# Optimization experiments

Measured on AMD Instinct MI355X. Metric: run time of the kernel, lower is better.

The kernel has to match this reference:

```python
import jax, jax.numpy as jnp
import numpy as np

N, S, C, K, V = 8, 2048, 4, 512, 64


def setup_inputs() -> dict:
    key = jax.random.key(0)
    kx, ke = jax.random.split(key)
    x = jax.random.normal(kx, (N, S, C, V), dtype=jnp.float32)
    # nn.Parameter(torch.rand(...)) -> uniform [0,1)
    embedding = jax.random.uniform(ke, (C, K, V), dtype=jnp.float32)
    return {"x": x, "embedding": embedding}


def reference(x, embedding):
    n, s, c, v = x.shape
    xf = x.reshape(n * s, c, v)  # (NS, C, V)
    x2 = jnp.sum(xf * xf, axis=-1, keepdims=True)           # (NS, C, 1)
    e2 = jnp.sum(embedding * embedding, axis=-1)            # (C, K)
    xe = jnp.einsum('ncv,ckv->nck', xf, embedding)          # (NS, C, K)
    d2 = x2 - 2.0 * xe + e2[None]                           # (NS, C, K)
    index = jnp.argmin(d2, axis=2)                          # (NS, C)
    # gather: output[n, c] = embedding[c, index[n, c]]
    output = embedding[jnp.arange(c)[None, :], index]       # (NS, C, V)
    output = output.reshape(x.shape)
    out0 = jax.lax.stop_gradient(output - x) + x            # straight-through
    d1 = jax.lax.stop_gradient(x) - output
    out1 = jnp.sum(d1 * d1, axis=3)                         # (N, S, C)
    d2_ = x - jax.lax.stop_gradient(output)
    out2 = jnp.sum(d2_ * d2_, axis=3)                       # (N, S, C)
    return (out0, out1, out2)
```

## Files before the change

kernel.cpp:

```cpp
#include <hip/hip_runtime.h>

#define NROW 16384
#define CCH  4
#define KCB  512
#define VDIM 64

typedef __attribute__((ext_vector_type(8))) short  short8;
typedef __attribute__((ext_vector_type(4))) float  floatx4;

__device__ inline unsigned short bf16h(float v, float* rem) {
    unsigned u = __float_as_uint(v);
    unsigned r = u + 0x7FFFu + ((u >> 16) & 1u);
    unsigned short h = (unsigned short)(r >> 16);
    *rem = v - __uint_as_float((unsigned)h << 16);
    return h;
}
__device__ inline unsigned short bf16r(float v) {
    unsigned u = __float_as_uint(v);
    return (unsigned short)((u + 0x7FFFu + ((u >> 16) & 1u)) >> 16);
}

__global__ __launch_bounds__(512, 4)
void vq_fused(const float* __restrict__ x, const float* __restrict__ emb,
              float* __restrict__ out) {
    extern __shared__ unsigned short smem[];
    unsigned short* eh = smem;
    float* e2s = (float*)(smem + 32768);
    float* pkm = e2s + KCB;

    const int tid  = threadIdx.x;
    const int lane = tid & 63;
    const int m    = lane & 15;
    const int quad = lane >> 4;
    const int wave = tid >> 6;
    const int c    = blockIdx.y;
    const int blockRow = blockIdx.x * 128;

    const float* embc = emb + (size_t)c * (KCB * VDIM);

    {
        const int cb = wave * 64;
        const int koct = m >> 1, half = m & 1;
#pragma unroll
        for (int j = 0; j < 16; ++j) {
            const int g = cb * 16 + j * 64 + lane;
            const float4 t = ((const float4*)embc)[g];
            const int code = cb + j * 4 + quad;
            ushort4 h4;
            h4.x = bf16r(t.x); h4.y = bf16r(t.y);
            h4.z = bf16r(t.z); h4.w = bf16r(t.w);
            const int off = (koct * 512 + (code ^ koct)) * 8 + half * 4;
            *(ushort4*)&eh[off] = h4;
            float s = 0.f;
            s = fmaf(t.x, t.x, s); s = fmaf(t.y, t.y, s);
            s = fmaf(t.z, t.z, s); s = fmaf(t.w, t.w, s);
            s += __shfl_xor(s, 1, 64);
            s += __shfl_xor(s, 2, 64);
            s += __shfl_xor(s, 4, 64);
            s += __shfl_xor(s, 8, 64);
            if (m == 0) e2s[code] = s;
        }
    }

    const int kh  = wave >> 2;
    const int rb2 = blockRow + (wave & 3) * 32;
    short8 ah[2][2], al[2][2];
#pragma unroll
    for (int rg = 0; rg < 2; ++rg) {
        const int row = rb2 + rg * 16 + m;
        const float4* xr = (const float4*)(x + ((size_t)row * CCH + c) * VDIM);
#pragma unroll
        for (int h = 0; h < 2; ++h) {
            const float4 f0 = xr[h * 8 + quad * 2];
            const float4 f1 = xr[h * 8 + quad * 2 + 1];
            const float fv[8] = {f0.x, f0.y, f0.z, f0.w, f1.x, f1.y, f1.z, f1.w};
            short8 hh, ll;
#pragma unroll
            for (int j = 0; j < 8; ++j) {
                float r, d;
                hh[j] = (short)bf16h(fv[j], &r);
                ll[j] = (short)bf16h(r, &d);
            }
            ah[rg][h] = hh; al[rg][h] = ll;
        }
    }

    __syncthreads();

    float pk0[4], pk1[4];
#pragma unroll
    for (int j = 0; j < 4; ++j) {
        pk0[j] = __uint_as_float(0x7F7FFFFFu);
        pk1[j] = __uint_as_float(0x7F7FFFFFu);
    }

    const int mq0 = m ^ quad;
    const int mq1 = m ^ (quad + 4);
    const int codeLane = kh * 256 + m;

#pragma unroll 2
    for (int t = 0; t < 16; ++t) {
        const int tt = kh * 16 + t;
        const short8 bh0 = *(const short8*)&eh[( quad      * 512 + tt * 16 + mq0) * 8];
        const short8 bh1 = *(const short8*)&eh[((quad + 4) * 512 + tt * 16 + mq1) * 8];
        const float e2v = e2s[tt * 16 + m];
        const int  code = codeLane + t * 16;

        floatx4 a0 = {0.f,0.f,0.f,0.f}, a1 = {0.f,0.f,0.f,0.f};
        a0 = __builtin_amdgcn_mfma_f32_16x16x32_bf16(ah[0][0], bh0, a0, 0, 0, 0);
        a1 = __builtin_amdgcn_mfma_f32_16x16x32_bf16(ah[1][0], bh0, a1, 0, 0, 0);
        a0 = __builtin_amdgcn_mfma_f32_16x16x32_bf16(al[0][0], bh0, a0, 0, 0, 0);
        a1 = __builtin_amdgcn_mfma_f32_16x16x32_bf16(al[1][0], bh0, a1, 0, 0, 0);
        a0 = __builtin_amdgcn_mfma_f32_16x16x32_bf16(ah[0][1], bh1, a0, 0, 0, 0);
        a1 = __builtin_amdgcn_mfma_f32_16x16x32_bf16(ah[1][1], bh1, a1, 0, 0, 0);
        a0 = __builtin_amdgcn_mfma_f32_16x16x32_bf16(al[0][1], bh1, a0, 0, 0, 0);
        a1 = __builtin_amdgcn_mfma_f32_16x16x32_bf16(al[1][1], bh1, a1, 0, 0, 0);

#pragma unroll
        for (int j = 0; j < 4; ++j) {
            const float d0 = fmaf(-2.0f, a0[j], e2v);
            pk0[j] = fminf(pk0[j],
                __uint_as_float((__float_as_uint(d0) & 0xFFFFFE00u) | code));
            const float d1 = fmaf(-2.0f, a1[j], e2v);
            pk1[j] = fminf(pk1[j],
                __uint_as_float((__float_as_uint(d1) & 0xFFFFFE00u) | code));
        }
    }

#pragma unroll
    for (int j = 0; j < 4; ++j) {
#pragma unroll
        for (int mask = 1; mask < 16; mask <<= 1) {
            pk0[j] = fminf(pk0[j], __shfl_xor(pk0[j], mask, 64));
            pk1[j] = fminf(pk1[j], __shfl_xor(pk1[j], mask, 64));
        }
    }

    {
        const int rloc = (wave & 3) * 32;
#pragma unroll
        for (int j = 0; j < 4; ++j) {
            if (m == j) {
                pkm[(rloc + quad * 4 + j) * 2 + kh]      = pk0[j];
                pkm[(rloc + 16 + quad * 4 + j) * 2 + kh] = pk1[j];
            }
        }
    }

    __syncthreads();

    const size_t base1 = (size_t)NROW * CCH * VDIM;
    const size_t base2 = base1 + (size_t)NROW * CCH;
#pragma unroll
    for (int j = 0; j < 4; ++j) {
        const int rl   = wave * 16 + quad * 4 + j;
        const float pmin = fminf(pkm[rl * 2], pkm[rl * 2 + 1]);
        const int  code  = (int)(__float_as_uint(pmin) & 511u);
        const int  row   = blockRow + rl;
        const float4 t4 = ((const float4*)(x + ((size_t)row * CCH + c) * VDIM))[m];
        const float4 e4 = ((const float4*)(embc + (size_t)code * VDIM))[m];
        float4 w;
        w.x = (e4.x - t4.x) + t4.x;
        w.y = (e4.y - t4.y) + t4.y;
        w.z = (e4.z - t4.z) + t4.z;
        w.w = (e4.w - t4.w) + t4.w;
        ((float4*)(out + ((size_t)row * CCH + c) * VDIM))[m] = w;
        float s = 0.f, dx;
        dx = t4.x - e4.x; s = fmaf(dx, dx, s);
        dx = t4.y - e4.y; s = fmaf(dx, dx, s);
        dx = t4.z - e4.z; s = fmaf(dx, dx, s);
        dx = t4.w - e4.w; s = fmaf(dx, dx, s);
        s += __shfl_xor(s, 1, 64);
        s += __shfl_xor(s, 2, 64);
        s += __shfl_xor(s, 4, 64);
        s += __shfl_xor(s, 8, 64);
        if (m == 0) {
            const size_t idx = (size_t)row * CCH + c;
            out[base1 + idx] = s;
            out[base2 + idx] = s;
        }
    }
}

extern "C" void kernel_launch(void* const* d_in, const int* in_sizes, int n_in,
                              void* d_out, int out_size, void* d_ws, size_t ws_size,
                              hipStream_t stream) {
    const float* x   = (const float*)d_in[0];
    const float* emb = (const float*)d_in[1];
    float* out = (float*)d_out;
    const size_t lds_bytes = 65536u + 2048u + 1024u;
    vq_fused<<<dim3(NROW / 128, CCH), dim3(512), lds_bytes, stream>>>(x, emb, out);
}
```

Measured before the change: 85.28 us.

## Precompute bf16 swizzled codebook and norms in a separate pre-pass kernel

Adds a small kernel that converts the embedding codebook to bf16 in the swizzled LDS layout and computes the squared norms once per channel, writing them to the workspace. The main kernel then copies the ready layout straight into LDS instead of having all 512 blocks redo the conversion and shuffle reductions. This adds a second launch and a serial dependency, and the precompute grid is only 4 blocks, which could add latency.

Result: no change. 86.47 us (+1.4%).

```diff
diff --git a/kernel.cpp b/kernel.cpp
--- a/kernel.cpp
+++ b/kernel.cpp
@@ -20,9 +20,31 @@
     return (unsigned short)((u + 0x7FFFu + ((u >> 16) & 1u)) >> 16);
 }
 
+__global__ __launch_bounds__(512)
+void vq_precomp(const float* __restrict__ emb, unsigned short* __restrict__ ws) {
+    const int c = blockIdx.x;
+    const int k = threadIdx.x;
+    const float* er = emb + ((size_t)c * KCB + k) * VDIM;
+    unsigned short* wc = ws + (size_t)c * 32768;
+    float s = 0.f;
+#pragma unroll
+    for (int q = 0; q < 16; ++q) {
+        const float4 t = ((const float4*)er)[q];
+        ushort4 h4;
+        h4.x = bf16r(t.x); h4.y = bf16r(t.y);
+        h4.z = bf16r(t.z); h4.w = bf16r(t.w);
+        const int koct = q >> 1, half = q & 1;
+        *(ushort4*)&wc[(koct * 512 + (k ^ koct)) * 8 + half * 4] = h4;
+        s = fmaf(t.x, t.x, s); s = fmaf(t.y, t.y, s);
+        s = fmaf(t.z, t.z, s); s = fmaf(t.w, t.w, s);
+    }
+    ((float*)(ws + 4 * 32768))[c * 512 + k] = s;
+}
+
+template <int MODE>
 __global__ __launch_bounds__(512, 4)
 void vq_fused(const float* __restrict__ x, const float* __restrict__ emb,
-              float* __restrict__ out) {
+              const unsigned short* __restrict__ ws, float* __restrict__ out) {
     extern __shared__ unsigned short smem[];
     unsigned short* eh = smem;
     float* e2s = (float*)(smem + 32768);
@@ -38,7 +60,13 @@
 
     const float* embc = emb + (size_t)c * (KCB * VDIM);
 
-    {
+    if constexpr (MODE == 1) {
+        const short8* wsrc = (const short8*)(ws + (size_t)c * 32768);
+#pragma unroll
+        for (int r = 0; r < 8; ++r)
+            *(short8*)&eh[(r * 512 + tid) * 8] = wsrc[r * 512 + tid];
+        e2s[tid] = ((const float*)(ws + 4 * 32768))[c * 512 + tid];
+    } else {
         const int cb = wave * 64;
         const int koct = m >> 1, half = m & 1;
 #pragma unroll
@@ -189,5 +217,14 @@
     const float* emb = (const float*)d_in[1];
     float* out = (float*)d_out;
     const size_t lds_bytes = 65536u + 2048u + 1024u;
-    vq_fused<<<dim3(NROW / 128, CCH), dim3(512), lds_bytes, stream>>>(x, emb, out);
-}
+    const size_t ws_need = 4u * 32768u * 2u + 4u * 512u * 4u;
+    if (d_ws != nullptr && ws_size >= ws_need) {
+        unsigned short* ws = (unsigned short*)d_ws;
+        vq_precomp<<<dim3(CCH), dim3(512), 0, stream>>>(emb, ws);
+        vq_fused<1><<<dim3(NROW / 128, CCH), dim3(512), lds_bytes, stream>>>(
+            x, emb, ws, out);
+    } else {
+        vq_fused<0><<<dim3(NROW / 128, CCH), dim3(512), lds_bytes, stream>>>(
+            x, emb, nullptr, out);
+    }
+}
```

## Stage reconstructed x in LDS and use nontemporal loads/stores

Applied to the files above, without the earlier changes.

Instead of re-reading x from global memory in the epilogue, the kernel rebuilds x from the bf16 hi/lo split already held in registers and stages it in LDS (padded stride) for the distance computation. The straight-through output now stores the codebook vector directly, and x loads and all output stores use nontemporal hints. This removes a second global read of x, but it adds an extra barrier and LDS traffic. The reconstructed x carries only about 16 mantissa bits, so the distance outputs may differ slightly from the fp32 reference.

Measured after the change: 104.5 us. 22.6% more time.

```diff
diff --git a/kernel.cpp b/kernel.cpp
--- a/kernel.cpp
+++ b/kernel.cpp
@@ -18,6 +18,9 @@
 __device__ inline unsigned short bf16r(float v) {
     unsigned u = __float_as_uint(v);
     return (unsigned short)((u + 0x7FFFu + ((u >> 16) & 1u)) >> 16);
+}
+__device__ inline float bf16f(short v) {
+    return __uint_as_float(((unsigned)(unsigned short)v) << 16);
 }
 
 __global__ __launch_bounds__(512, 4)
@@ -68,11 +71,11 @@
 #pragma unroll
     for (int rg = 0; rg < 2; ++rg) {
         const int row = rb2 + rg * 16 + m;
-        const float4* xr = (const float4*)(x + ((size_t)row * CCH + c) * VDIM);
+        const floatx4* xr = (const floatx4*)(x + ((size_t)row * CCH + c) * VDIM);
 #pragma unroll
         for (int h = 0; h < 2; ++h) {
-            const float4 f0 = xr[h * 8 + quad * 2];
-            const float4 f1 = xr[h * 8 + quad * 2 + 1];
+            const floatx4 f0 = __builtin_nontemporal_load(xr + h * 8 + quad * 2);
+            const floatx4 f1 = __builtin_nontemporal_load(xr + h * 8 + quad * 2 + 1);
             const float fv[8] = {f0.x, f0.y, f0.z, f0.w, f1.x, f1.y, f1.z, f1.w};
             short8 hh, ll;
 #pragma unroll
@@ -149,6 +152,31 @@
 
     __syncthreads();
 
+    {
+        floatx4* xs4 = (floatx4*)smem;
+        if (kh == 0) {
+#pragma unroll
+            for (int rg = 0; rg < 2; ++rg) {
+                const int lr = (wave & 3) * 32 + rg * 16 + m;
+#pragma unroll
+                for (int h = 0; h < 2; ++h) {
+#pragma unroll
+                    for (int hf = 0; hf < 2; ++hf) {
+                        floatx4 v;
+                        v.x = bf16f(ah[rg][h][hf * 4 + 0]) + bf16f(al[rg][h][hf * 4 + 0]);
+                        v.y = bf16f(ah[rg][h][hf * 4 + 1]) + bf16f(al[rg][h][hf * 4 + 1]);
+                        v.z = bf16f(ah[rg][h][hf * 4 + 2]) + bf16f(al[rg][h][hf * 4 + 2]);
+                        v.w = bf16f(ah[rg][h][hf * 4 + 3]) + bf16f(al[rg][h][hf * 4 + 3]);
+                        xs4[lr * 17 + h * 8 + quad * 2 + hf] = v;
+                    }
+                }
+            }
+        }
+    }
+
+    __syncthreads();
+
+    const floatx4* xs4 = (const floatx4*)smem;
     const size_t base1 = (size_t)NROW * CCH * VDIM;
     const size_t base2 = base1 + (size_t)NROW * CCH;
 #pragma unroll
@@ -157,14 +185,10 @@
         const float pmin = fminf(pkm[rl * 2], pkm[rl * 2 + 1]);
         const int  code  = (int)(__float_as_uint(pmin) & 511u);
         const int  row   = blockRow + rl;
-        const float4 t4 = ((const float4*)(x + ((size_t)row * CCH + c) * VDIM))[m];
-        const float4 e4 = ((const float4*)(embc + (size_t)code * VDIM))[m];
-        float4 w;
-        w.x = (e4.x - t4.x) + t4.x;
-        w.y = (e4.y - t4.y) + t4.y;
-        w.z = (e4.z - t4.z) + t4.z;
-        w.w = (e4.w - t4.w) + t4.w;
-        ((float4*)(out + ((size_t)row * CCH + c) * VDIM))[m] = w;
+        const floatx4 t4 = xs4[rl * 17 + m];
+        const floatx4 e4 = ((const floatx4*)(embc + (size_t)code * VDIM))[m];
+        __builtin_nontemporal_store(
+            e4, (floatx4*)(out + ((size_t)row * CCH + c) * VDIM) + m);
         float s = 0.f, dx;
         dx = t4.x - e4.x; s = fmaf(dx, dx, s);
         dx = t4.y - e4.y; s = fmaf(dx, dx, s);
@@ -176,8 +200,8 @@
         s += __shfl_xor(s, 8, 64);
         if (m == 0) {
             const size_t idx = (size_t)row * CCH + c;
-            out[base1 + idx] = s;
-            out[base2 + idx] = s;
+            __builtin_nontemporal_store(s, &out[base1 + idx]);
+            __builtin_nontemporal_store(s, &out[base2 + idx]);
         }
     }
 }
```

## Split codebook across blocks with atomicMin argmin, separate epilogue kernel

Applied to the files above, without the earlier changes.

Splits the argmin into a kernel whose grid also spans two codebook halves. Each block loads only half the embedding into LDS, halving the LDS footprint and allowing more resident blocks. Partial minima are merged with atomicMin on an order-preserving key in a workspace, and a second kernel gathers the chosen codes and writes the outputs with coalesced row-wide access. This adds a memset, two extra launches, atomic traffic and a second read of x, and falls back to the old fused kernel when no workspace is available.

After: 88.71 us. 1.04x slower.

```diff
diff --git a/kernel.cpp b/kernel.cpp
--- a/kernel.cpp
+++ b/kernel.cpp
@@ -20,13 +20,12 @@
     return (unsigned short)((u + 0x7FFFu + ((u >> 16) & 1u)) >> 16);
 }
 
-__global__ __launch_bounds__(512, 4)
-void vq_fused(const float* __restrict__ x, const float* __restrict__ emb,
-              float* __restrict__ out) {
+__global__ __launch_bounds__(512, 8)
+void vq_argmin(const float* __restrict__ x, const float* __restrict__ emb,
+               unsigned int* __restrict__ ws) {
     extern __shared__ unsigned short smem[];
     unsigned short* eh = smem;
-    float* e2s = (float*)(smem + 32768);
-    float* pkm = e2s + KCB;
+    float* e2s = (float*)(smem + 16384);
 
     const int tid  = threadIdx.x;
     const int lane = tid & 63;
@@ -34,22 +33,23 @@
     const int quad = lane >> 4;
     const int wave = tid >> 6;
     const int c    = blockIdx.y;
+    const int half = blockIdx.z;
     const int blockRow = blockIdx.x * 128;
 
-    const float* embc = emb + (size_t)c * (KCB * VDIM);
+    const float* embh = emb + ((size_t)c * KCB + (size_t)half * 256) * VDIM;
 
     {
-        const int cb = wave * 64;
-        const int koct = m >> 1, half = m & 1;
-#pragma unroll
-        for (int j = 0; j < 16; ++j) {
+        const int cb = wave * 32;
+        const int koct = m >> 1, hlf = m & 1;
+#pragma unroll
+        for (int j = 0; j < 8; ++j) {
             const int g = cb * 16 + j * 64 + lane;
-            const float4 t = ((const float4*)embc)[g];
+            const float4 t = ((const float4*)embh)[g];
             const int code = cb + j * 4 + quad;
             ushort4 h4;
             h4.x = bf16r(t.x); h4.y = bf16r(t.y);
             h4.z = bf16r(t.z); h4.w = bf16r(t.w);
-            const int off = (koct * 512 + (code ^ koct)) * 8 + half * 4;
+            const int off = (koct * 256 + (code ^ koct)) * 8 + hlf * 4;
             *(ushort4*)&eh[off] = h4;
             float s = 0.f;
             s = fmaf(t.x, t.x, s); s = fmaf(t.y, t.y, s);
@@ -62,6 +62,150 @@
         }
     }
 
+    short8 ah[2], al[2];
+    {
+        const int row = blockRow + wave * 16 + m;
+        const float4* xr = (const float4*)(x + ((size_t)row * CCH + c) * VDIM);
+#pragma unroll
+        for (int h = 0; h < 2; ++h) {
+            const float4 f0 = xr[h * 8 + quad * 2];
+            const float4 f1 = xr[h * 8 + quad * 2 + 1];
+            const float fv[8] = {f0.x, f0.y, f0.z, f0.w, f1.x, f1.y, f1.z, f1.w};
+            short8 hh, ll;
+#pragma unroll
+            for (int j = 0; j < 8; ++j) {
+                float r, d;
+                hh[j] = (short)bf16h(fv[j], &r);
+                ll[j] = (short)bf16h(r, &d);
+            }
+            ah[h] = hh; al[h] = ll;
+        }
+    }
+
+    __syncthreads();
+
+    float pk[4];
+#pragma unroll
+    for (int j = 0; j < 4; ++j) pk[j] = __uint_as_float(0x7F7FFFFFu);
+
+    const int mq0 = m ^ quad;
+    const int mq1 = m ^ (quad + 4);
+    const int codeLane = half * 256 + m;
+
+#pragma unroll 2
+    for (int t = 0; t < 16; ++t) {
+        const short8 bh0 = *(const short8*)&eh[( quad      * 256 + t * 16 + mq0) * 8];
+        const short8 bh1 = *(const short8*)&eh[((quad + 4) * 256 + t * 16 + mq1) * 8];
+        const float e2v = e2s[t * 16 + m];
+        const int  code = codeLane + t * 16;
+
+        floatx4 a0 = {0.f,0.f,0.f,0.f}, a1 = {0.f,0.f,0.f,0.f};
+        a0 = __builtin_amdgcn_mfma_f32_16x16x32_bf16(ah[0], bh0, a0, 0, 0, 0);
+        a1 = __builtin_amdgcn_mfma_f32_16x16x32_bf16(ah[1], bh1, a1, 0, 0, 0);
+        a0 = __builtin_amdgcn_mfma_f32_16x16x32_bf16(al[0], bh0, a0, 0, 0, 0);
+        a1 = __builtin_amdgcn_mfma_f32_16x16x32_bf16(al[1], bh1, a1, 0, 0, 0);
+
+#pragma unroll
+        for (int j = 0; j < 4; ++j) {
+            const float d0 = fmaf(-2.0f, a0[j] + a1[j], e2v);
+            pk[j] = fminf(pk[j],
+                __uint_as_float((__float_as_uint(d0) & 0xFFFFFE00u) | code));
+        }
+    }
+
+#pragma unroll
+    for (int j = 0; j < 4; ++j) {
+#pragma unroll
+        for (int mask = 1; mask < 16; mask <<= 1)
+            pk[j] = fminf(pk[j], __shfl_xor(pk[j], mask, 64));
+    }
+
+#pragma unroll
+    for (int j = 0; j < 4; ++j) {
+        if (m == j) {
+            const int row = blockRow + wave * 16 + quad * 4 + j;
+            const unsigned u = __float_as_uint(pk[j]);
+            const unsigned key = (u >> 31) ? ~u : (u | 0x80000000u);
+            atomicMin(&ws[row * CCH + c], key);
+        }
+    }
+}
+
+__global__ __launch_bounds__(512)
+void vq_epilogue(const float* __restrict__ x, const float* __restrict__ emb,
+                 const unsigned int* __restrict__ ws, float* __restrict__ out) {
+    const int lane = threadIdx.x & 63;
+    const int wave = threadIdx.x >> 6;
+    const int row  = blockIdx.x * 8 + wave;
+    const int c    = lane >> 4;
+    const int m    = lane & 15;
+
+    const unsigned key  = ws[row * CCH + c];
+    const unsigned code = ((key >> 31) ? key : ~key) & 511u;
+
+    const floatx4 e4 = ((const floatx4*)(emb + ((size_t)c * KCB + code) * VDIM))[m];
+    const floatx4 t4 = ((const floatx4*)(x   + (size_t)row * (CCH * VDIM)))[lane];
+    ((floatx4*)(out + (size_t)row * (CCH * VDIM)))[lane] = e4;
+
+    float s = 0.f, dx;
+    dx = t4.x - e4.x; s = fmaf(dx, dx, s);
+    dx = t4.y - e4.y; s = fmaf(dx, dx, s);
+    dx = t4.z - e4.z; s = fmaf(dx, dx, s);
+    dx = t4.w - e4.w; s = fmaf(dx, dx, s);
+    s += __shfl_xor(s, 1, 64);
+    s += __shfl_xor(s, 2, 64);
+    s += __shfl_xor(s, 4, 64);
+    s += __shfl_xor(s, 8, 64);
+
+    const float v0 = __shfl(s,  0, 64);
+    const float v1 = __shfl(s, 16, 64);
+    const float v2 = __shfl(s, 32, 64);
+    const float v3 = __shfl(s, 48, 64);
+    if (lane == 0) {
+        const size_t base1 = (size_t)NROW * CCH * VDIM;
+        floatx4 o = {v0, v1, v2, v3};
+        *(floatx4*)(out + base1 + (size_t)row * CCH) = o;
+        *(floatx4*)(out + base1 + (size_t)NROW * CCH + (size_t)row * CCH) = o;
+    }
+}
+
+__global__ __launch_bounds__(512, 4)
+void vq_mono(const float* __restrict__ x, const float* __restrict__ emb,
+             float* __restrict__ out) {
+    extern __shared__ unsigned short smem[];
+    unsigned short* eh = smem;
+    float* e2s = (float*)(smem + 32768);
+    float* pkm = e2s + KCB;
+
+    const int tid  = threadIdx.x;
+    const int lane = tid & 63;
+    const int m    = lane & 15;
+    const int quad = lane >> 4;
+    const int wave = tid >> 6;
+    const int c    = blockIdx.y;
+    const int blockRow = blockIdx.x * 128;
+    const float* embc = emb + (size_t)c * (KCB * VDIM);
+
+    {
+        const int cb = wave * 64;
+        const int koct = m >> 1, hlf = m & 1;
+#pragma unroll
+        for (int j = 0; j < 16; ++j) {
+            const int g = cb * 16 + j * 64 + lane;
+            const float4 t = ((const float4*)embc)[g];
+            const int code = cb + j * 4 + quad;
+            ushort4 h4;
+            h4.x = bf16r(t.x); h4.y = bf16r(t.y);
+            h4.z = bf16r(t.z); h4.w = bf16r(t.w);
+            *(ushort4*)&eh[(koct * 512 + (code ^ koct)) * 8 + hlf * 4] = h4;
+            float s = 0.f;
+            s = fmaf(t.x, t.x, s); s = fmaf(t.y, t.y, s);
+            s = fmaf(t.z, t.z, s); s = fmaf(t.w, t.w, s);
+            s += __shfl_xor(s, 1, 64); s += __shfl_xor(s, 2, 64);
+            s += __shfl_xor(s, 4, 64); s += __shfl_xor(s, 8, 64);
+            if (m == 0) e2s[code] = s;
+        }
+    }
     const int kh  = wave >> 2;
     const int rb2 = blockRow + (wave & 3) * 32;
     short8 ah[2][2], al[2][2];
@@ -84,20 +228,15 @@
             ah[rg][h] = hh; al[rg][h] = ll;
         }
     }
-
     __syncthreads();
-
     float pk0[4], pk1[4];
 #pragma unroll
     for (int j = 0; j < 4; ++j) {
         pk0[j] = __uint_as_float(0x7F7FFFFFu);
         pk1[j] = __uint_as_float(0x7F7FFFFFu);
     }
-
-    const int mq0 = m ^ quad;
-    const int mq1 = m ^ (quad + 4);
+    const int mq0 = m ^ quad, mq1 = m ^ (quad + 4);
     const int codeLane = kh * 256 + m;
-
 #pragma unroll 2
     for (int t = 0; t < 16; ++t) {
         const int tt = kh * 16 + t;
@@ -105,7 +244,6 @@
         const short8 bh1 = *(const short8*)&eh[((quad + 4) * 512 + tt * 16 + mq1) * 8];
         const float e2v = e2s[tt * 16 + m];
         const int  code = codeLane + t * 16;
-
         floatx4 a0 = {0.f,0.f,0.f,0.f}, a1 = {0.f,0.f,0.f,0.f};
         a0 = __builtin_amdgcn_mfma_f32_16x16x32_bf16(ah[0][0], bh0, a0, 0, 0, 0);
         a1 = __builtin_amdgcn_mfma_f32_16x16x32_bf16(ah[1][0], bh0, a1, 0, 0, 0);
@@ -115,18 +253,14 @@
         a1 = __builtin_amdgcn_mfma_f32_16x16x32_bf16(ah[1][1], bh1, a1, 0, 0, 0);
         a0 = __builtin_amdgcn_mfma_f32_16x16x32_bf16(al[0][1], bh1, a0, 0, 0, 0);
         a1 = __builtin_amdgcn_mfma_f32_16x16x32_bf16(al[1][1], bh1, a1, 0, 0, 0);
-
 #pragma unroll
         for (int j = 0; j < 4; ++j) {
             const float d0 = fmaf(-2.0f, a0[j], e2v);
-            pk0[j] = fminf(pk0[j],
-                __uint_as_float((__float_as_uint(d0) & 0xFFFFFE00u) | code));
+            pk0[j] = fminf(pk0[j], __uint_as_float((__float_as_uint(d0) & 0xFFFFFE00u) | code));
             const float d1 = fmaf(-2.0f, a1[j], e2v);
-            pk1[j] = fminf(pk1[j],
-                __uint_as_float((__float_as_uint(d1) & 0xFFFFFE00u) | code));
-        }
-    }
-
+            pk1[j] = fminf(pk1[j], __uint_as_float((__float_as_uint(d1) & 0xFFFFFE00u) | code));
+        }
+    }
 #pragma unroll
     for (int j = 0; j < 4; ++j) {
 #pragma unroll
@@ -135,7 +269,6 @@
             pk1[j] = fminf(pk1[j], __shfl_xor(pk1[j], mask, 64));
         }
     }
-
     {
         const int rloc = (wave & 3) * 32;
 #pragma unroll
@@ -146,9 +279,7 @@
             }
         }
     }
-
     __syncthreads();
-
     const size_t base1 = (size_t)NROW * CCH * VDIM;
     const size_t base2 = base1 + (size_t)NROW * CCH;
 #pragma unroll
@@ -160,20 +291,16 @@
         const float4 t4 = ((const float4*)(x + ((size_t)row * CCH + c) * VDIM))[m];
         const float4 e4 = ((const float4*)(embc + (size_t)code * VDIM))[m];
         float4 w;
-        w.x = (e4.x - t4.x) + t4.x;
-        w.y = (e4.y - t4.y) + t4.y;
-        w.z = (e4.z - t4.z) + t4.z;
-        w.w = (e4.w - t4.w) + t4.w;
+        w.x = (e4.x - t4.x) + t4.x; w.y = (e4.y - t4.y) + t4.y;
+        w.z = (e4.z - t4.z) + t4.z; w.w = (e4.w - t4.w) + t4.w;
         ((float4*)(out + ((size_t)row * CCH + c) * VDIM))[m] = w;
         float s = 0.f, dx;
         dx = t4.x - e4.x; s = fmaf(dx, dx, s);
         dx = t4.y - e4.y; s = fmaf(dx, dx, s);
         dx = t4.z - e4.z; s = fmaf(dx, dx, s);
         dx = t4.w - e4.w; s = fmaf(dx, dx, s);
-        s += __shfl_xor(s, 1, 64);
-        s += __shfl_xor(s, 2, 64);
-        s += __shfl_xor(s, 4, 64);
-        s += __shfl_xor(s, 8, 64);
+        s += __shfl_xor(s, 1, 64); s += __shfl_xor(s, 2, 64);
+        s += __shfl_xor(s, 4, 64); s += __shfl_xor(s, 8, 64);
         if (m == 0) {
             const size_t idx = (size_t)row * CCH + c;
             out[base1 + idx] = s;
@@ -188,6 +315,15 @@
     const float* x   = (const float*)d_in[0];
     const float* emb = (const float*)d_in[1];
     float* out = (float*)d_out;
-    const size_t lds_bytes = 65536u + 2048u + 1024u;
-    vq_fused<<<dim3(NROW / 128, CCH), dim3(512), lds_bytes, stream>>>(x, emb, out);
-}
+    const size_t ws_need = (size_t)NROW * CCH * sizeof(unsigned int);
+    if (d_ws != nullptr && ws_size >= ws_need) {
+        unsigned int* ws = (unsigned int*)d_ws;
+        hipMemsetAsync(ws, 0xFF, ws_need, stream);
+        vq_argmin<<<dim3(NROW / 128, CCH, 2), dim3(512),
+                    32768u + 1024u, stream>>>(x, emb, ws);
+        vq_epilogue<<<dim3(NROW / 8), dim3(512), 0, stream>>>(x, emb, ws, out);
+    } else {
+        vq_mono<<<dim3(NROW / 128, CCH), dim3(512),
+                  65536u + 2048u + 1024u, stream>>>(x, emb, out);
+    }
+}
```
